# Optimization experiments

Measured on AMD Instinct MI355X. Metric: run time of the kernel, lower is better.

## Reference

```python
import jax, jax.numpy as jnp
import numpy as np

B, N, D_IN, D_ATTN, D_OUT = 8, 2048, 2048, 64, 2048

def setup_inputs() -> dict:
    key = jax.random.key(0)
    ks = jax.random.split(key, 5)
    x = jax.random.normal(ks[0], (B, N, D_IN), dtype=jnp.float32)
    s_qkv = 1.0 / np.sqrt(D_IN)   # torch nn.Linear default init bound
    W_qkv = jax.random.uniform(ks[1], (D_IN, 3 * D_ATTN), jnp.float32, -s_qkv, s_qkv)
    b_qkv = jax.random.uniform(ks[2], (3 * D_ATTN,), jnp.float32, -s_qkv, s_qkv)
    s_p = 1.0 / np.sqrt(D_ATTN)
    W_proj = jax.random.uniform(ks[3], (D_ATTN, D_OUT), jnp.float32, -s_p, s_p)
    b_proj = jax.random.uniform(ks[4], (D_OUT,), jnp.float32, -s_p, s_p)
    return {"x": x, "W_qkv": W_qkv, "b_qkv": b_qkv, "W_proj": W_proj, "b_proj": b_proj}

def reference(x, W_qkv, b_qkv, W_proj, b_proj):
    # qkv projection: [B,N,3*D_ATTN]
    qkv = x @ W_qkv + b_qkv
    q, k, v = jnp.split(qkv, 3, axis=-1)  # each [B,N,D_ATTN]
    scale = jax.lax.rsqrt(jnp.float32(D_ATTN))
    w = jnp.einsum('bnd,bmd->bnm', q, k) * scale  # [B,N,N]
    a = jax.nn.softmax(w, axis=-1)
    ctx = jnp.einsum('bnm,bmd->bnd', a, v)        # [B,N,D_ATTN]
    return ctx @ W_proj + b_proj                   # [B,N,D_OUT]
```

## Files before the change

kernel.cpp:

```cpp
#include <hip/hip_runtime.h>

typedef __bf16 bf16x8 __attribute__((ext_vector_type(8)));
typedef unsigned short u16x8 __attribute__((ext_vector_type(8)));
typedef unsigned short u16x4 __attribute__((ext_vector_type(4)));
typedef float  f32x4  __attribute__((ext_vector_type(4)));

#define QSCALE 0.1803368801111204f

__device__ __forceinline__ unsigned short f2bf(float f) {
  unsigned int u = __float_as_uint(f);
  u = u + 0x7fffu + ((u >> 16) & 1u);
  return (unsigned short)(u >> 16);
}

#define GLD16(src, dst)                                                        \
  __builtin_amdgcn_global_load_lds(                                            \
      (const __attribute__((address_space(1))) void*)(src),                    \
      (__attribute__((address_space(3))) void*)(dst), 16, 0, 0)


__global__ __launch_bounds__(256) void k_trw(const float* __restrict__ Wq,
                                             const float* __restrict__ Wp,
                                             unsigned short* __restrict__ wqT,
                                             unsigned short* __restrict__ wpT) {
  __shared__ float tile[64][193];
  const int t = threadIdx.x;
  if (blockIdx.x < 32) {
    const int k0 = blockIdx.x * 64;
#pragma unroll
    for (int i = 0; i < 12; ++i) {
      int u = i * 256 + t;
      int row = u / 48, c4 = u % 48;
      float4 v = *(const float4*)(Wq + (size_t)(k0 + row) * 192 + c4 * 4);
      tile[row][c4 * 4 + 0] = v.x; tile[row][c4 * 4 + 1] = v.y;
      tile[row][c4 * 4 + 2] = v.z; tile[row][c4 * 4 + 3] = v.w;
    }
    __syncthreads();
#pragma unroll
    for (int i = 0; i < 6; ++i) {
      int u = i * 256 + t;
      int c = u >> 3, k8 = (u & 7) * 8;
      u16x8 h;
#pragma unroll
      for (int j = 0; j < 8; ++j) h[j] = f2bf(tile[k8 + j][c]);
      *(u16x8*)(wqT + (size_t)c * 2048 + k0 + k8) = h;
    }
  } else {
    const int n0 = (blockIdx.x - 32) * 64;
#pragma unroll
    for (int i = 0; i < 4; ++i) {
      int u = i * 256 + t;
      int dd = u >> 4, c4 = u & 15;
      float4 v = *(const float4*)(Wp + (size_t)dd * 2048 + n0 + c4 * 4);
      tile[dd][c4 * 4 + 0] = v.x; tile[dd][c4 * 4 + 1] = v.y;
      tile[dd][c4 * 4 + 2] = v.z; tile[dd][c4 * 4 + 3] = v.w;
    }
    __syncthreads();
#pragma unroll
    for (int i = 0; i < 2; ++i) {
      int u = i * 256 + t;
      int n = u >> 3, d8 = (u & 7) * 8;
      u16x8 h;
      h[0] = f2bf(tile[d8 + 0][n]); h[1] = f2bf(tile[d8 + 1][n]);
      h[2] = f2bf(tile[d8 + 2][n]); h[3] = f2bf(tile[d8 + 3][n]);
      h[4] = f2bf(tile[d8 + 4][n]); h[5] = f2bf(tile[d8 + 5][n]);
      h[6] = f2bf(tile[d8 + 6][n]); h[7] = f2bf(tile[d8 + 7][n]);
      *(u16x8*)(wpT + (size_t)(n0 + n) * 64 + d8) = h;
    }
  }
}

__global__ __launch_bounds__(512) void k_qkv(const float* __restrict__ x,
                                             const unsigned short* __restrict__ wqT,
                                             const float* __restrict__ b_qkv,
                                             unsigned short* __restrict__ qb,
                                             unsigned short* __restrict__ kb,
                                             unsigned short* __restrict__ vt) {
  __shared__ __align__(16) char lds[65536];
  const int t = threadIdx.x;
  const int lane = t & 63, w = t >> 6;
  const int l15 = lane & 15, l4 = lane >> 4;
  const int wm = w >> 2, wn = w & 3;
  const int m0 = blockIdx.x * 64;

  const int arow = t >> 3;
  const int akc  = (t & 7) * 8;
  const float* xrow = x + (size_t)(m0 + arow) * 2048 + akc;
  const int aoff = arow * 128 + ((akc * 2) ^ ((arow & 7) << 4));

  f32x4 acc[2][3] = {};
  float4 xa0_0, xa1_0, xa0_1, xa1_1;

  auto issueA_0 = [&](int kt) {
    xa0_0 = *(const float4*)(xrow + kt * 64);
    xa1_0 = *(const float4*)(xrow + kt * 64 + 4);
  };
  auto issueA_1 = [&](int kt) {
    xa0_1 = *(const float4*)(xrow + kt * 64);
    xa1_1 = *(const float4*)(xrow + kt * 64 + 4);
  };
  auto writeA_0 = [&]() {
    u16x8 h;
    h[0] = f2bf(xa0_0.x); h[1] = f2bf(xa0_0.y); h[2] = f2bf(xa0_0.z); h[3] = f2bf(xa0_0.w);
    h[4] = f2bf(xa1_0.x); h[5] = f2bf(xa1_0.y); h[6] = f2bf(xa1_0.z); h[7] = f2bf(xa1_0.w);
    *(u16x8*)(lds + 0 * 8192 + aoff) = h;
  };
  auto writeA_1 = [&]() {
    u16x8 h;
    h[0] = f2bf(xa0_1.x); h[1] = f2bf(xa0_1.y); h[2] = f2bf(xa0_1.z); h[3] = f2bf(xa0_1.w);
    h[4] = f2bf(xa1_1.x); h[5] = f2bf(xa1_1.y); h[6] = f2bf(xa1_1.z); h[7] = f2bf(xa1_1.w);
    *(u16x8*)(lds + 1 * 8192 + aoff) = h;
  };
  auto stageB = [&](int kt, int d) {
    char* bbase = lds + 16384 + d * 24576;
#pragma unroll
    for (int p = 0; p < 3; ++p) {
      int L = p * 8192 + (w << 10) + (lane << 4);
      int row = L >> 7;
      int cb = (L & 127) ^ ((row & 7) << 4);
      GLD16((const char*)wqT + (size_t)row * 4096 + kt * 128 + cb,
            bbase + p * 8192 + (w << 10));
    }
  };
  auto compute = [&](int d) {
    const char* aB = lds + d * 8192;
    const char* bB = lds + 16384 + d * 24576;
    __builtin_amdgcn_s_setprio(1);
#pragma unroll
    for (int kk = 0; kk < 2; ++kk) {
      int cb = kk * 64 + l4 * 16;
      bf16x8 af[2], bfr[3];
#pragma unroll
      for (int m = 0; m < 2; ++m) {
        int r = wm * 32 + m * 16 + l15;
        af[m] = *(const bf16x8*)(aB + r * 128 + (cb ^ ((r & 7) << 4)));
      }
#pragma unroll
      for (int n = 0; n < 3; ++n) {
        int r = wn * 48 + n * 16 + l15;
        bfr[n] = *(const bf16x8*)(bB + r * 128 + (cb ^ ((r & 7) << 4)));
      }
#pragma unroll
      for (int m = 0; m < 2; ++m)
#pragma unroll
        for (int n = 0; n < 3; ++n)
          acc[m][n] = __builtin_amdgcn_mfma_f32_16x16x32_bf16(af[m], bfr[n], acc[m][n], 0, 0, 0);
    }
    __builtin_amdgcn_s_setprio(0);
  };

#define QKV_STEP(n, P, DOI, DOS, W)                                    \
  {                                                                    \
    writeA_##P();                                                      \
    __builtin_amdgcn_sched_barrier(0);                                 \
    if (DOS) stageB((n) + 1, (P) ^ 1);                                 \
    __builtin_amdgcn_sched_barrier(0);                                 \
    if (DOI) issueA_##P((n) + 2);                                      \
    asm volatile("s_waitcnt vmcnt(" W ") lgkmcnt(0)" ::: "memory");    \
    __builtin_amdgcn_s_barrier();                                      \
    compute(P);                                                        \
    __builtin_amdgcn_s_barrier();                                      \
  }

  stageB(0, 0);
  __builtin_amdgcn_sched_barrier(0);
  issueA_0(0); issueA_1(1);
  for (int kt = 0; kt < 30; kt += 2) {
    QKV_STEP(kt,     0, true, true, "7");
    QKV_STEP(kt + 1, 1, true, true, "7");
  }
  QKV_STEP(30, 0, false, true,  "5");
  QKV_STEP(31, 1, false, false, "0");
#undef QKV_STEP

#pragma unroll
  for (int m = 0; m < 2; ++m)
#pragma unroll
    for (int n = 0; n < 3; ++n) {
      int c = wn * 48 + n * 16 + l15;
      int j = c >> 6, cc = c & 63;
      float bias = b_qkv[c];
      int grow0 = m0 + wm * 32 + m * 16 + l4 * 4;
      if (j == 0) {
#pragma unroll
        for (int r = 0; r < 4; ++r)
          qb[(size_t)(grow0 + r) * 64 + cc] = f2bf((acc[m][n][r] + bias) * QSCALE);
      } else if (j == 1) {
#pragma unroll
        for (int r = 0; r < 4; ++r)
          kb[(size_t)(grow0 + r) * 64 + cc] = f2bf(acc[m][n][r] + bias);
      } else {
        int bbv = grow0 >> 11, nn0 = grow0 & 2047;
        u16x4 h;
        h[0] = f2bf(acc[m][n][0] + bias); h[1] = f2bf(acc[m][n][1] + bias);
        h[2] = f2bf(acc[m][n][2] + bias); h[3] = f2bf(acc[m][n][3] + bias);
        *(u16x4*)(vt + ((size_t)bbv * 64 + cc) * 2048 + nn0) = h;
      }
    }
}

#define P_CTX1 0
#define P_ML1  16384
#define P_SA   24576
#define P_BIAS 32768
#define P_WPT  40960
__global__ __launch_bounds__(512) void k_attnproj(const unsigned short* __restrict__ qb,
                                                  const unsigned short* __restrict__ kb,
                                                  const unsigned short* __restrict__ vt,
                                                  const unsigned short* __restrict__ wpT,
                                                  const float* __restrict__ b_proj,
                                                  float* __restrict__ out) {
  __shared__ __align__(16) char lds[73728];
  const int t = threadIdx.x;
  const int lane = t & 63, w = t >> 6;
  const int l15 = lane & 15, l4 = lane >> 4;
  const int wq = w & 3, wh = w >> 2;
  const int lin = blockIdx.x;
  const int bb = lin & 7;
  const int qbase = (lin >> 3) * 64;
  const int q0 = qbase + wq * 16;
  const int kt0 = wh * 16;
  const unsigned short* qrow = qb + ((size_t)bb * 2048 + q0 + l15) * 64;
  bf16x8 aq[2];
  aq[0] = *(const bf16x8*)(qrow + l4 * 8);
  aq[1] = *(const bf16x8*)(qrow + 32 + l4 * 8);
  f32x4 ctx[4] = {};
  float m = -1e30f, lsum = 0.f;
  const char* kBase = (const char*)kb + (size_t)bb * 2048 * 128;
  const char* vBase = (const char*)vt + (size_t)bb * 64 * 4096;
  const int srcA = ((l4 & 1) << 5) | l15;
  const int srcB = srcA + 16;
  const bool hi = (l4 >> 1) & 1;

  auto stage = [&](int kt, int d) {
#pragma unroll
    for (int p = 0; p < 2; ++p) {
      int L = p * 4096 + (wq << 10) + (lane << 4);
      int row = L >> 7;
      int cb = (L & 127) ^ ((row & 7) << 4);
      GLD16(kBase + (size_t)(kt * 64 + row) * 128 + cb,
            lds + wh * 32768 + d * 8192 + p * 4096 + (wq << 10));
      GLD16(vBase + (size_t)row * 4096 + kt * 128 + cb,
            lds + wh * 32768 + 16384 + d * 8192 + p * 4096 + (wq << 10));
    }
  };
  auto stageB = [&](int c, int dd) {
    char* bbase = lds + P_WPT + dd * 16384;
#pragma unroll
    for (int p = 0; p < 2; ++p) {
      int L = p * 8192 + t * 16;
      int row = L >> 7;
      int cb = (L & 127) ^ ((row & 7) << 4);
      GLD16((const char*)wpT + (size_t)(c * 128 + row) * 128 + cb,
            bbase + p * 8192 + (w << 10));
    }
  };

  stage(kt0, 0);
  int d = 0;
  for (int kt = 0; kt < 16; ++kt) {
    if (kt < 15) {
      stage(kt0 + kt + 1, d ^ 1);
      asm volatile("s_waitcnt vmcnt(4)" ::: "memory");
    } else {
      asm volatile("s_waitcnt vmcnt(0)" ::: "memory");
    }
    __builtin_amdgcn_s_barrier();
    const char* sK = lds + wh * 32768 + d * 8192;
    const char* sV = lds + wh * 32768 + 16384 + d * 8192;
    f32x4 s[4] = {};
    __builtin_amdgcn_s_setprio(1);
#pragma unroll
    for (int kk = 0; kk < 2; ++kk) {
      int cb = kk * 64 + l4 * 16;
#pragma unroll
      for (int mf = 0; mf < 4; ++mf) {
        int r = mf * 16 + l15;
        bf16x8 kf = *(const bf16x8*)(sK + r * 128 + (cb ^ ((r & 7) << 4)));
        s[mf] = __builtin_amdgcn_mfma_f32_16x16x32_bf16(kf, aq[kk], s[mf], 0, 0, 0);
      }
    }
    __builtin_amdgcn_s_setprio(0);
    float t0 = fmaxf(fmaxf(s[0][0], s[0][1]), s[0][2]);
    float t1 = fmaxf(fmaxf(s[0][3], s[1][0]), s[1][1]);
    float t2 = fmaxf(fmaxf(s[1][2], s[1][3]), s[2][0]);
    float t3 = fmaxf(fmaxf(s[2][1], s[2][2]), s[2][3]);
    float t4 = fmaxf(fmaxf(s[3][0], s[3][1]), s[3][2]);
    float pm = fmaxf(fmaxf(fmaxf(t0, t1), t2), fmaxf(fmaxf(t3, t4), s[3][3]));
    pm = fmaxf(pm, __shfl_xor(pm, 16));
    pm = fmaxf(pm, __shfl_xor(pm, 32));
    if (!__all(pm <= m + 11.5f)) {
      float mn = fmaxf(m, pm);
      float al = __builtin_exp2f(m - mn);
      m = mn; lsum *= al;
#pragma unroll
      for (int df = 0; df < 4; ++df)
#pragma unroll
        for (int r = 0; r < 4; ++r) ctx[df][r] *= al;
    }
    float lp = 0.f;
#pragma unroll
    for (int mf = 0; mf < 4; ++mf)
#pragma unroll
      for (int r = 0; r < 4; ++r) {
        float p = __builtin_exp2f(s[mf][r] - m);
        s[mf][r] = p;
        lp += p;
      }
    lsum += lp;
    unsigned int pk[4][2];
#pragma unroll
    for (int mf = 0; mf < 4; ++mf) {
      asm("v_cvt_pk_bf16_f32 %0, %1, %2" : "=v"(pk[mf][0]) : "v"(s[mf][0]), "v"(s[mf][1]));
      asm("v_cvt_pk_bf16_f32 %0, %1, %2" : "=v"(pk[mf][1]) : "v"(s[mf][2]), "v"(s[mf][3]));
    }
#pragma unroll
    for (int kk = 0; kk < 2; ++kk) {
      unsigned int q00 = __shfl((int)pk[2 * kk][0], srcA);
      unsigned int q10 = __shfl((int)pk[2 * kk + 1][0], srcA);
      unsigned int q01 = __shfl((int)pk[2 * kk][1], srcA);
      unsigned int q11 = __shfl((int)pk[2 * kk + 1][1], srcA);
      unsigned int r00 = __shfl((int)pk[2 * kk][0], srcB);
      unsigned int r10 = __shfl((int)pk[2 * kk + 1][0], srcB);
      unsigned int r01 = __shfl((int)pk[2 * kk][1], srcB);
      unsigned int r11 = __shfl((int)pk[2 * kk + 1][1], srcB);
      uint4 uu;
      uu.x = hi ? q10 : q00;
      uu.y = hi ? q11 : q01;
      uu.z = hi ? r10 : r00;
      uu.w = hi ? r11 : r01;
      bf16x8 pfrag = *(bf16x8*)&uu;
      int cb = kk * 64 + l4 * 16;
      __builtin_amdgcn_s_setprio(1);
#pragma unroll
      for (int df = 0; df < 4; ++df) {
        int rv = df * 16 + l15;
        bf16x8 vf = *(const bf16x8*)(sV + rv * 128 + (cb ^ ((rv & 7) << 4)));
        ctx[df] = __builtin_amdgcn_mfma_f32_16x16x32_bf16(vf, pfrag, ctx[df], 0, 0, 0);
      }
      __builtin_amdgcn_s_setprio(0);
    }
    __builtin_amdgcn_s_barrier();
    d ^= 1;
  }
  lsum += __shfl_xor(lsum, 16);
  lsum += __shfl_xor(lsum, 32);

  GLD16((const char*)b_proj + (w << 10) + (lane << 4), lds + P_BIAS + (w << 10));
  stageB(0, 0); stageB(1, 1);

  if (wh == 1) {
    char* cbase = lds + P_CTX1 + (wq << 12);
#pragma unroll
    for (int df = 0; df < 4; ++df) {
      int byte = l15 * 256 + df * 64 + l4 * 16;
      *(f32x4*)(cbase + (byte ^ ((l15 & 7) << 4))) = ctx[df];
    }
    if (l4 == 0)
      *(float2*)(lds + P_ML1 + wq * 128 + l15 * 8) = make_float2(m, lsum);
  }
  asm volatile("s_waitcnt lgkmcnt(0)" ::: "memory");
  __builtin_amdgcn_sched_barrier(0);
  __builtin_amdgcn_s_barrier();
  if (wh == 0) {
    char* cbase = lds + P_CTX1 + (wq << 12);
    float2 ml1 = *(const float2*)(lds + P_ML1 + wq * 128 + l15 * 8);
    float M = fmaxf(m, ml1.x);
    float a0 = __builtin_exp2f(m - M), a1 = __builtin_exp2f(ml1.x - M);
    float inv = 1.0f / (lsum * a0 + ml1.y * a1);
    a0 *= inv; a1 *= inv;
    int rq = wq * 16 + l15;
#pragma unroll
    for (int df = 0; df < 4; ++df) {
      int byte = l15 * 256 + df * 64 + l4 * 16;
      f32x4 c1 = *(const f32x4*)(cbase + (byte ^ ((l15 & 7) << 4)));
      u16x4 h;
      h[0] = f2bf(ctx[df][0] * a0 + c1[0] * a1);
      h[1] = f2bf(ctx[df][1] * a0 + c1[1] * a1);
      h[2] = f2bf(ctx[df][2] * a0 + c1[2] * a1);
      h[3] = f2bf(ctx[df][3] * a0 + c1[3] * a1);
      int sbyte = rq * 128 + ((df * 32 + l4 * 8) ^ ((rq & 7) << 4));
      *(u16x4*)(lds + P_SA + sbyte) = h;
    }
  }
  asm volatile("s_waitcnt lgkmcnt(0)" ::: "memory");
  __builtin_amdgcn_sched_barrier(0);
  __builtin_amdgcn_s_barrier();

#pragma unroll
  for (int c = 0; c < 16; ++c) {
    if (c == 0)       asm volatile("s_waitcnt vmcnt(2) lgkmcnt(0)" ::: "memory");
    else if (c == 15) asm volatile("s_waitcnt vmcnt(4) lgkmcnt(0)" ::: "memory");
    else              asm volatile("s_waitcnt vmcnt(6) lgkmcnt(0)" ::: "memory");
    __builtin_amdgcn_s_barrier();
    const char* bB = lds + P_WPT + (c & 1) * 16384;
    f32x4 acc[4] = {};
    __builtin_amdgcn_s_setprio(1);
#pragma unroll
    for (int kk = 0; kk < 2; ++kk) {
      int cb = kk * 64 + l4 * 16;
      bf16x8 af[4], bfr;
#pragma unroll
      for (int mm = 0; mm < 4; ++mm) {
        int r = mm * 16 + l15;
        af[mm] = *(const bf16x8*)(lds + P_SA + r * 128 + (cb ^ ((r & 7) << 4)));
      }
      {
        int r = w * 16 + l15;
        bfr = *(const bf16x8*)(bB + r * 128 + (cb ^ ((r & 7) << 4)));
      }
#pragma unroll
      for (int mm = 0; mm < 4; ++mm)
        acc[mm] = __builtin_amdgcn_mfma_f32_16x16x32_bf16(bfr, af[mm], acc[mm], 0, 0, 0);
    }
    __builtin_amdgcn_s_setprio(0);
#pragma unroll
    for (int mm = 0; mm < 4; ++mm) {
      int grow = qbase + mm * 16 + l15;
      int gcol = c * 128 + w * 16 + l4 * 4;
      float4 bias = *(const float4*)(lds + P_BIAS + gcol * 4);
      float4 o;
      o.x = acc[mm][0] + bias.x; o.y = acc[mm][1] + bias.y;
      o.z = acc[mm][2] + bias.z; o.w = acc[mm][3] + bias.w;
      *(float4*)(out + ((size_t)bb * 2048 + grow) * 2048 + gcol) = o;
    }
    __builtin_amdgcn_s_barrier();
    if (c < 14) stageB(c + 2, c & 1);
  }
}

extern "C" void kernel_launch(void* const* d_in, const int* in_sizes, int n_in,
                              void* d_out, int out_size, void* d_ws, size_t ws_size,
                              hipStream_t stream) {
  const float* x      = (const float*)d_in[0];
  const float* W_qkv  = (const float*)d_in[1];
  const float* b_qkv  = (const float*)d_in[2];
  const float* W_proj = (const float*)d_in[3];
  const float* b_proj = (const float*)d_in[4];
  float* out = (float*)d_out;

  unsigned short* ws   = (unsigned short*)d_ws;
  unsigned short* wqT  = ws;
  unsigned short* wpT  = wqT + (size_t)192 * 2048;
  unsigned short* qb   = wpT + (size_t)2048 * 64;
  unsigned short* kb   = qb  + (size_t)16384 * 64;
  unsigned short* vt   = kb  + (size_t)16384 * 64;

  k_trw<<<64, 256, 0, stream>>>(W_qkv, W_proj, wqT, wpT);
  k_qkv<<<256, 512, 0, stream>>>(x, wqT, b_qkv, qb, kb, vt);
  k_attnproj<<<256, 512, 0, stream>>>(qb, kb, vt, wpT, b_proj, out);
}
```

Before: 91.81 us.

## Halve QKV GEMM row tile to 32 rows and double grid size

Reduces the QKV projection block tile from 64 to 32 rows, so each thread loads one float4 of x per k-step and each wave computes one 16-row MFMA tile. The grid doubles to 512 blocks and LDS per block shrinks, aiming for better CU occupancy and more memory parallelism on the bandwidth-bound x read. The trade-off is that the weight tile is restaged twice as often, and each LDS B-fragment read feeds fewer MFMAs.

Result: slower. 102.3 us (+11.4%).

```diff
diff --git a/kernel.cpp b/kernel.cpp
--- a/kernel.cpp
+++ b/kernel.cpp
@@ -76,43 +76,35 @@
                                              unsigned short* __restrict__ qb,
                                              unsigned short* __restrict__ kb,
                                              unsigned short* __restrict__ vt) {
-  __shared__ __align__(16) char lds[65536];
+  __shared__ __align__(16) char lds[57344];
   const int t = threadIdx.x;
   const int lane = t & 63, w = t >> 6;
   const int l15 = lane & 15, l4 = lane >> 4;
   const int wm = w >> 2, wn = w & 3;
-  const int m0 = blockIdx.x * 64;
-
-  const int arow = t >> 3;
-  const int akc  = (t & 7) * 8;
+  const int m0 = blockIdx.x * 32;
+
+  const int arow = t >> 4;
+  const int akc  = (t & 15) * 4;
   const float* xrow = x + (size_t)(m0 + arow) * 2048 + akc;
   const int aoff = arow * 128 + ((akc * 2) ^ ((arow & 7) << 4));
 
-  f32x4 acc[2][3] = {};
-  float4 xa0_0, xa1_0, xa0_1, xa1_1;
-
-  auto issueA_0 = [&](int kt) {
-    xa0_0 = *(const float4*)(xrow + kt * 64);
-    xa1_0 = *(const float4*)(xrow + kt * 64 + 4);
-  };
-  auto issueA_1 = [&](int kt) {
-    xa0_1 = *(const float4*)(xrow + kt * 64);
-    xa1_1 = *(const float4*)(xrow + kt * 64 + 4);
-  };
+  f32x4 acc[1][3] = {};
+  float4 xa_0, xa_1;
+
+  auto issueA_0 = [&](int kt) { xa_0 = *(const float4*)(xrow + kt * 64); };
+  auto issueA_1 = [&](int kt) { xa_1 = *(const float4*)(xrow + kt * 64); };
   auto writeA_0 = [&]() {
-    u16x8 h;
-    h[0] = f2bf(xa0_0.x); h[1] = f2bf(xa0_0.y); h[2] = f2bf(xa0_0.z); h[3] = f2bf(xa0_0.w);
-    h[4] = f2bf(xa1_0.x); h[5] = f2bf(xa1_0.y); h[6] = f2bf(xa1_0.z); h[7] = f2bf(xa1_0.w);
-    *(u16x8*)(lds + 0 * 8192 + aoff) = h;
+    u16x4 h;
+    h[0] = f2bf(xa_0.x); h[1] = f2bf(xa_0.y); h[2] = f2bf(xa_0.z); h[3] = f2bf(xa_0.w);
+    *(u16x4*)(lds + 0 * 4096 + aoff) = h;
   };
   auto writeA_1 = [&]() {
-    u16x8 h;
-    h[0] = f2bf(xa0_1.x); h[1] = f2bf(xa0_1.y); h[2] = f2bf(xa0_1.z); h[3] = f2bf(xa0_1.w);
-    h[4] = f2bf(xa1_1.x); h[5] = f2bf(xa1_1.y); h[6] = f2bf(xa1_1.z); h[7] = f2bf(xa1_1.w);
-    *(u16x8*)(lds + 1 * 8192 + aoff) = h;
+    u16x4 h;
+    h[0] = f2bf(xa_1.x); h[1] = f2bf(xa_1.y); h[2] = f2bf(xa_1.z); h[3] = f2bf(xa_1.w);
+    *(u16x4*)(lds + 1 * 4096 + aoff) = h;
   };
   auto stageB = [&](int kt, int d) {
-    char* bbase = lds + 16384 + d * 24576;
+    char* bbase = lds + 8192 + d * 24576;
 #pragma unroll
     for (int p = 0; p < 3; ++p) {
       int L = p * 8192 + (w << 10) + (lane << 4);
@@ -123,17 +115,16 @@
     }
   };
   auto compute = [&](int d) {
-    const char* aB = lds + d * 8192;
-    const char* bB = lds + 16384 + d * 24576;
+    const char* aB = lds + d * 4096;
+    const char* bB = lds + 8192 + d * 24576;
     __builtin_amdgcn_s_setprio(1);
 #pragma unroll
     for (int kk = 0; kk < 2; ++kk) {
       int cb = kk * 64 + l4 * 16;
-      bf16x8 af[2], bfr[3];
-#pragma unroll
-      for (int m = 0; m < 2; ++m) {
-        int r = wm * 32 + m * 16 + l15;
-        af[m] = *(const bf16x8*)(aB + r * 128 + (cb ^ ((r & 7) << 4)));
+      bf16x8 af, bfr[3];
+      {
+        int r = wm * 16 + l15;
+        af = *(const bf16x8*)(aB + r * 128 + (cb ^ ((r & 7) << 4)));
       }
 #pragma unroll
       for (int n = 0; n < 3; ++n) {
@@ -141,10 +132,8 @@
         bfr[n] = *(const bf16x8*)(bB + r * 128 + (cb ^ ((r & 7) << 4)));
       }
 #pragma unroll
-      for (int m = 0; m < 2; ++m)
-#pragma unroll
-        for (int n = 0; n < 3; ++n)
-          acc[m][n] = __builtin_amdgcn_mfma_f32_16x16x32_bf16(af[m], bfr[n], acc[m][n], 0, 0, 0);
+      for (int n = 0; n < 3; ++n)
+        acc[0][n] = __builtin_amdgcn_mfma_f32_16x16x32_bf16(af, bfr[n], acc[0][n], 0, 0, 0);
     }
     __builtin_amdgcn_s_setprio(0);
   };
@@ -166,37 +155,35 @@
   __builtin_amdgcn_sched_barrier(0);
   issueA_0(0); issueA_1(1);
   for (int kt = 0; kt < 30; kt += 2) {
-    QKV_STEP(kt,     0, true, true, "7");
-    QKV_STEP(kt + 1, 1, true, true, "7");
-  }
-  QKV_STEP(30, 0, false, true,  "5");
+    QKV_STEP(kt,     0, true, true, "5");
+    QKV_STEP(kt + 1, 1, true, true, "5");
+  }
+  QKV_STEP(30, 0, false, true,  "4");
   QKV_STEP(31, 1, false, false, "0");
 #undef QKV_STEP
 
 #pragma unroll
-  for (int m = 0; m < 2; ++m)
-#pragma unroll
-    for (int n = 0; n < 3; ++n) {
-      int c = wn * 48 + n * 16 + l15;
-      int j = c >> 6, cc = c & 63;
-      float bias = b_qkv[c];
-      int grow0 = m0 + wm * 32 + m * 16 + l4 * 4;
-      if (j == 0) {
-#pragma unroll
-        for (int r = 0; r < 4; ++r)
-          qb[(size_t)(grow0 + r) * 64 + cc] = f2bf((acc[m][n][r] + bias) * QSCALE);
-      } else if (j == 1) {
-#pragma unroll
-        for (int r = 0; r < 4; ++r)
-          kb[(size_t)(grow0 + r) * 64 + cc] = f2bf(acc[m][n][r] + bias);
-      } else {
-        int bbv = grow0 >> 11, nn0 = grow0 & 2047;
-        u16x4 h;
-        h[0] = f2bf(acc[m][n][0] + bias); h[1] = f2bf(acc[m][n][1] + bias);
-        h[2] = f2bf(acc[m][n][2] + bias); h[3] = f2bf(acc[m][n][3] + bias);
-        *(u16x4*)(vt + ((size_t)bbv * 64 + cc) * 2048 + nn0) = h;
-      }
-    }
+  for (int n = 0; n < 3; ++n) {
+    int c = wn * 48 + n * 16 + l15;
+    int j = c >> 6, cc = c & 63;
+    float bias = b_qkv[c];
+    int grow0 = m0 + wm * 16 + l4 * 4;
+    if (j == 0) {
+#pragma unroll
+      for (int r = 0; r < 4; ++r)
+        qb[(size_t)(grow0 + r) * 64 + cc] = f2bf((acc[0][n][r] + bias) * QSCALE);
+    } else if (j == 1) {
+#pragma unroll
+      for (int r = 0; r < 4; ++r)
+        kb[(size_t)(grow0 + r) * 64 + cc] = f2bf(acc[0][n][r] + bias);
+    } else {
+      int bbv = grow0 >> 11, nn0 = grow0 & 2047;
+      u16x4 h;
+      h[0] = f2bf(acc[0][n][0] + bias); h[1] = f2bf(acc[0][n][1] + bias);
+      h[2] = f2bf(acc[0][n][2] + bias); h[3] = f2bf(acc[0][n][3] + bias);
+      *(u16x4*)(vt + ((size_t)bbv * 64 + cc) * 2048 + nn0) = h;
+    }
+  }
 }
 
 #define P_CTX1 0
@@ -447,6 +434,6 @@
   unsigned short* vt   = kb  + (size_t)16384 * 64;
 
   k_trw<<<64, 256, 0, stream>>>(W_qkv, W_proj, wqT, wpT);
-  k_qkv<<<256, 512, 0, stream>>>(x, wqT, b_qkv, qb, kb, vt);
+  k_qkv<<<512, 512, 0, stream>>>(x, wqT, b_qkv, qb, kb, vt);
   k_attnproj<<<256, 512, 0, stream>>>(qb, kb, vt, wpT, b_proj, out);
 }
```
